# Performance work log

Hardware: AMD Instinct MI355X
Metric: run time of the kernel (lower is better)

The kernel has to match this reference:

```python
import jax, jax.numpy as jnp
import numpy as np

H, W, C = 56, 56, 384
WS, SHIFT, HEADS = 7, 3, 12
HEAD_DIM = C // HEADS
SCALE = HEAD_DIM ** (-0.5)
NWIN = (H // WS) * (W // WS)  # 64 windows per image
NTOK = WS * WS                # 49 tokens per window
EPS = 1e-5


def _gen_mask():
    # static shift-window attention mask, computed with numpy (jit-safe constant)
    img = np.zeros((H, W))
    sl = (slice(0, -WS), slice(-WS, -SHIFT), slice(-SHIFT, None))
    cnt = 0
    for hs in sl:
        for ws in sl:
            img[hs, ws] = cnt
            cnt += 1
    mw = img.reshape(H // WS, WS, W // WS, WS).transpose(0, 2, 1, 3).reshape(-1, NTOK)
    diff = mw[:, None, :] - mw[:, :, None]  # (NWIN, NTOK, NTOK)
    return jnp.asarray(np.where(diff != 0, -100.0, 0.0), dtype=jnp.float32)

ATTN_MASK = _gen_mask()


def _layernorm(x, g, b):
    mu = jnp.mean(x, axis=-1, keepdims=True)
    var = jnp.var(x, axis=-1, keepdims=True)
    return (x - mu) * jax.lax.rsqrt(var + EPS) * g + b


def setup_inputs() -> dict:
    key = jax.random.key(0)
    ks = jax.random.split(key, 6)
    s = 0.02
    return {
        "x": jax.random.normal(ks[0], (16, H * W, C), dtype=jnp.float32),
        "ln1_g": jnp.ones((C,), jnp.float32),
        "ln1_b": jnp.zeros((C,), jnp.float32),
        "qkv_w": jax.random.normal(ks[1], (C, 3 * C), jnp.float32) * s,
        "proj_w": jax.random.normal(ks[2], (C, C), jnp.float32) * s,
        "proj_b": jnp.zeros((C,), jnp.float32),
        "ln2_g": jnp.ones((C,), jnp.float32),
        "ln2_b": jnp.zeros((C,), jnp.float32),
        "fc1_w": jax.random.normal(ks[3], (C, 4 * C), jnp.float32) * s,
        "fc1_b": jnp.zeros((4 * C,), jnp.float32),
        "fc2_w": jax.random.normal(ks[4], (4 * C, C), jnp.float32) * s,
        "fc2_b": jnp.zeros((C,), jnp.float32),
    }


def reference(x, ln1_g, ln1_b, qkv_w, proj_w, proj_b, ln2_g, ln2_b, fc1_w, fc1_b, fc2_w, fc2_b):
    B, N, _ = x.shape
    h = x
    y = _layernorm(x, ln1_g, ln1_b).reshape(B, H, W, C)
    # cyclic shift (note: source never rolls back; we match it)
    y = jnp.roll(y, shift=(-SHIFT, -SHIFT), axis=(1, 2))
    # window partition -> (B*NWIN, NTOK, C)
    y = y.reshape(B, H // WS, WS, W // WS, WS, C).transpose(0, 1, 3, 2, 4, 5)
    y = y.reshape(B * NWIN, NTOK, C)
    # qkv (no bias), split heads
    qkv = (y @ qkv_w).reshape(B * NWIN, NTOK, 3, HEADS, HEAD_DIM)
    qkv = qkv.transpose(2, 0, 3, 1, 4)  # (3, BW, heads, NTOK, hd)
    q, k, v = qkv[0], qkv[1], qkv[2]
    attn = jnp.einsum('whnd,whmd->whnm', q, k) * SCALE  # (BW, heads, NTOK, NTOK)
    attn = attn.reshape(B, NWIN, HEADS, NTOK, NTOK) + ATTN_MASK[None, :, None]
    attn = jax.nn.softmax(attn.reshape(B * NWIN, HEADS, NTOK, NTOK), axis=-1)
    o = jnp.einsum('whnm,whmd->whnd', attn, v)
    o = o.transpose(0, 2, 1, 3).reshape(B * NWIN, NTOK, C)
    o = o @ proj_w + proj_b
    # window reverse -> (B, N, C)
    o = o.reshape(B, H // WS, W // WS, WS, WS, C).transpose(0, 1, 3, 2, 4, 5)
    o = o.reshape(B, N, C)
    x1 = h + o
    # MLP (GELU after both fc1 and fc2, as in source)
    m = _layernorm(x1, ln2_g, ln2_b)
    m = jax.nn.gelu(m @ fc1_w + fc1_b, approximate=False)
    m = jax.nn.gelu(m @ fc2_w + fc2_b, approximate=False)
    return x1 + m
```

## Files before the change

kernel.cpp:

```cpp
#include <hip/hip_runtime.h>
#include <hip/hip_bf16.h>
#include <cstdint>
#include <cstddef>

#define C_DIM   384
#define NIMG    3136
#define MROWS   50176
#define QK_SCALE 0.17677669529663687f

using bf16x8 = __attribute__((ext_vector_type(8))) short;
using f32x4  = __attribute__((ext_vector_type(4))) float;

__device__ __forceinline__ short f2bf(float f) {
  union { float f; uint32_t u; } v; v.f = f;
  uint32_t r = (v.u + 0x7fffu + ((v.u >> 16) & 1u)) >> 16;
  return (short)(uint16_t)r;
}

__device__ __forceinline__ float bf2f(short s) {
  union { uint32_t u; float f; } v; v.u = ((uint32_t)(uint16_t)s) << 16;
  return v.f;
}

__device__ __forceinline__ void async_copy16(const void* g, void* l) {
  __builtin_amdgcn_global_load_lds(
      (const __attribute__((address_space(1))) void*)g,
      (__attribute__((address_space(3))) void*)l, 16, 0, 0);
}

__device__ __forceinline__ float gelu_fast(float x) {
  float x2 = x * x;
  float u = fmaf(0.0356774081f, x2, 0.7978845608f);
  float e = exp2f(x * u * 2.8853900818f);
  float r = __builtin_amdgcn_rcpf(e + 1.0f);
  return fmaf(-x, r, x);
}

__global__ __launch_bounds__(256) void transpose_cast(
    const float* __restrict__ w, short* __restrict__ wt, int K, int N) {
  int idx = blockIdx.x * 256 + threadIdx.x;
  if (idx >= K * N) return;
  int k = idx / N;
  int n = idx - k * N;
  wt[(size_t)n * K + k] = f2bf(w[idx]);
}

template <typename IN>
__global__ __launch_bounds__(256) void ln_kernel(
    const IN* __restrict__ x, const float* __restrict__ g,
    const float* __restrict__ b, short* __restrict__ y, int windowed) {
  int token = blockIdx.x * 4 + (threadIdx.x >> 6);
  int lane = threadIdx.x & 63;
  size_t src;
  if (windowed) {
    int bw = token / 49;
    int tt = token - bw * 49;
    int bb = bw >> 6, w = bw & 63;
    int hs = (w >> 3) * 7 + tt / 7 + 3; if (hs >= 56) hs -= 56;
    int ws = (w & 7) * 7 + (tt % 7) + 3; if (ws >= 56) ws -= 56;
    src = (size_t)(bb * NIMG + hs * 56 + ws) * C_DIM;
  } else {
    src = (size_t)token * C_DIM;
  }
  const IN* xr = x + src;
  float v[6];
  float s = 0.f;
#pragma unroll
  for (int i = 0; i < 6; ++i) {
    if constexpr (sizeof(IN) == 4) v[i] = (float)xr[lane + i * 64];
    else v[i] = bf2f((short)xr[lane + i * 64]);
    s += v[i];
  }
#pragma unroll
  for (int m = 1; m < 64; m <<= 1) s += __shfl_xor(s, m);
  float mu = s * (1.0f / 384.0f);
  float var = 0.f;
#pragma unroll
  for (int i = 0; i < 6; ++i) { float d = v[i] - mu; var += d * d; }
#pragma unroll
  for (int m = 1; m < 64; m <<= 1) var += __shfl_xor(var, m);
  float rstd = rsqrtf(var * (1.0f / 384.0f) + 1e-5f);
  short* yr = y + (size_t)token * C_DIM;
#pragma unroll
  for (int i = 0; i < 6; ++i) {
    int c = lane + i * 64;
    yr[c] = f2bf((v[i] - mu) * rstd * g[c] + b[c]);
  }
}

template <int EPI>
__device__ __forceinline__ void gemm_epilogue(
    f32x4 (&acc)[4][4], void* Out, const float* bias, const void* resid,
    int N, int m0, int n0, int wm, int wn, int lrow, int quad) {
#pragma unroll
  for (int i = 0; i < 4; ++i) {
#pragma unroll
    for (int r = 0; r < 4; ++r) {
      int row = m0 + wm * 64 + i * 16 + quad * 4 + r;
      if (EPI == 1) {
        int bw = row / 49;
        int tt = row - bw * 49;
        int bb = bw >> 6, w = bw & 63;
        int nimg = ((w >> 3) * 7 + tt / 7) * 56 + (w & 7) * 7 + (tt % 7);
        size_t obase = ((size_t)(bb * NIMG + nimg)) * C_DIM;
#pragma unroll
        for (int j = 0; j < 4; ++j) {
          int col = n0 + wn * 64 + j * 16 + lrow;
          size_t oi = obase + col;
          ((short*)Out)[oi] =
              f2bf(acc[i][j][r] + bias[col] + ((const float*)resid)[oi]);
        }
      } else {
#pragma unroll
        for (int j = 0; j < 4; ++j) {
          int col = n0 + wn * 64 + j * 16 + lrow;
          float v = acc[i][j][r];
          if (EPI == 0) {
            ((short*)Out)[(size_t)row * N + col] = f2bf(v);
          } else if (EPI == 2) {
            ((short*)Out)[(size_t)row * N + col] = f2bf(gelu_fast(v + bias[col]));
          } else {
            size_t oi = (size_t)row * C_DIM + col;
            ((float*)Out)[oi] =
                bf2f(((const short*)resid)[oi]) + gelu_fast(v + bias[col]);
          }
        }
      }
    }
  }
}

__device__ __forceinline__ void grid_decode(int nby, int& m0, int& n0) {
  const int wg = (int)blockIdx.x;
  const int swz = (wg & 7) * ((int)gridDim.x >> 3) + (wg >> 3);
  const int mb = swz / nby;
  const int nb = swz - mb * nby;
  m0 = mb * 128;
  n0 = nb * 128;
}

template <int EPI>
__global__ __launch_bounds__(256, 4) void gemm_pipe32_kernel(
    const short* __restrict__ A, const short* __restrict__ Bt,
    void* __restrict__ Out, const float* __restrict__ bias,
    const void* __restrict__ resid, int M, int N, int K, int nby) {
  __shared__ __align__(16) short lds[2][128 * 32 * 2];
  const int t = threadIdx.x;
  const int wave = t >> 6, lane = t & 63;
  const int lrow = lane & 15, quad = lane >> 4;
  const int wm = wave & 1, wn = wave >> 1;
  int m0, n0;
  grid_decode(nby, m0, n0);

  f32x4 acc[4][4] = {};
  const int srow = t >> 2;
  const int spos = t & 3;
  const int nt = K >> 5;

  auto stage = [&](int buf, int k0) {
    short* la = &lds[buf][0];
    short* lb = la + 128 * 32;
#pragma unroll
    for (int i = 0; i < 2; ++i) {
      int row = i * 64 + srow;
      int ca = spos ^ ((row >> 1) & 3);
      async_copy16(A + (size_t)(m0 + row) * K + k0 + ca * 8,
                   la + (i * 64 + wave * 16) * 32);
      async_copy16(Bt + (size_t)(n0 + row) * K + k0 + ca * 8,
                   lb + (i * 64 + wave * 16) * 32);
    }
  };

  auto compute = [&](int buf) {
    short* ldsA = &lds[buf][0];
    short* ldsB = ldsA + 128 * 32;
    bf16x8 af[4], bfr[4];
#pragma unroll
    for (int i = 0; i < 4; ++i) {
      int ra = wm * 64 + i * 16 + lrow;
      af[i] = *(const bf16x8*)(ldsA + ra * 32 + ((quad ^ ((ra >> 1) & 3)) * 8));
      int rb = wn * 64 + i * 16 + lrow;
      bfr[i] = *(const bf16x8*)(ldsB + rb * 32 + ((quad ^ ((rb >> 1) & 3)) * 8));
    }
    __builtin_amdgcn_s_setprio(1);
#pragma unroll
    for (int i = 0; i < 4; ++i)
#pragma unroll
      for (int j = 0; j < 4; ++j)
        acc[i][j] = __builtin_amdgcn_mfma_f32_16x16x32_bf16(af[i], bfr[j],
                                                            acc[i][j], 0, 0, 0);
    __builtin_amdgcn_s_setprio(0);
  };

  stage(0, 0);
  for (int kt = 0; kt < nt; ++kt) {
    __builtin_amdgcn_sched_barrier(0);
    if (kt + 1 < nt) {
      stage((kt + 1) & 1, (kt + 1) * 32);
      asm volatile("s_waitcnt vmcnt(4)" ::: "memory");
    } else {
      asm volatile("s_waitcnt vmcnt(0)" ::: "memory");
    }
    __builtin_amdgcn_s_barrier();
    __builtin_amdgcn_sched_barrier(0);
    compute(kt & 1);
    __builtin_amdgcn_sched_barrier(0);
    __builtin_amdgcn_s_barrier();
  }
  gemm_epilogue<EPI>(acc, Out, bias, resid, N, m0, n0, wm, wn, lrow, quad);
}

template <int EPI>
__global__ __launch_bounds__(256, 2) void gemm_pipe64_kernel(
    const short* __restrict__ A, const short* __restrict__ Bt,
    void* __restrict__ Out, const float* __restrict__ bias,
    const void* __restrict__ resid, int M, int N, int K, int nby) {
  __shared__ __align__(16) short lds[2][128 * 64 * 2];
  const int t = threadIdx.x;
  const int wave = t >> 6, lane = t & 63;
  const int lrow = lane & 15, quad = lane >> 4;
  const int wm = wave & 1, wn = wave >> 1;
  int m0, n0;
  grid_decode(nby, m0, n0);

  f32x4 acc[4][4] = {};
  const int srow = t >> 3;
  const int spos = t & 7;
  const int nt = K >> 6;

  auto stage = [&](int buf, int k0) {
    short* la = &lds[buf][0];
    short* lb = la + 128 * 64;
#pragma unroll
    for (int i = 0; i < 4; ++i) {
      int row = i * 32 + srow;
      int ca = spos ^ (row & 7);
      async_copy16(A + (size_t)(m0 + row) * K + k0 + ca * 8,
                   la + (i * 32 + wave * 8) * 64);
      async_copy16(Bt + (size_t)(n0 + row) * K + k0 + ca * 8,
                   lb + (i * 32 + wave * 8) * 64);
    }
  };

  auto compute = [&](int buf) {
    short* ldsA = &lds[buf][0];
    short* ldsB = ldsA + 128 * 64;
#pragma unroll
    for (int ks = 0; ks < 2; ++ks) {
      const int cb = ks * 4;
      bf16x8 af[4], bfr[4];
#pragma unroll
      for (int i = 0; i < 4; ++i) {
        int ra = wm * 64 + i * 16 + lrow;
        af[i] = *(const bf16x8*)(ldsA + ra * 64 + (((cb + quad) ^ (ra & 7)) * 8));
        int rb = wn * 64 + i * 16 + lrow;
        bfr[i] = *(const bf16x8*)(ldsB + rb * 64 + (((cb + quad) ^ (rb & 7)) * 8));
      }
      __builtin_amdgcn_s_setprio(1);
#pragma unroll
      for (int i = 0; i < 4; ++i)
#pragma unroll
        for (int j = 0; j < 4; ++j)
          acc[i][j] = __builtin_amdgcn_mfma_f32_16x16x32_bf16(af[i], bfr[j],
                                                              acc[i][j], 0, 0, 0);
      __builtin_amdgcn_s_setprio(0);
    }
  };

  stage(0, 0);
  for (int kt = 0; kt < nt; ++kt) {
    __builtin_amdgcn_sched_barrier(0);
    if (kt + 1 < nt) {
      stage((kt + 1) & 1, (kt + 1) * 64);
      asm volatile("s_waitcnt vmcnt(8)" ::: "memory");
    } else {
      asm volatile("s_waitcnt vmcnt(0)" ::: "memory");
    }
    __builtin_amdgcn_s_barrier();
    __builtin_amdgcn_sched_barrier(0);
    compute(kt & 1);
    __builtin_amdgcn_sched_barrier(0);
    __builtin_amdgcn_s_barrier();
  }
  gemm_epilogue<EPI>(acc, Out, bias, resid, N, m0, n0, wm, wn, lrow, quad);
}

__global__ __launch_bounds__(256) void attn_kernel(
    const short* __restrict__ qkv, short* __restrict__ o) {
  __shared__ __align__(16) short plds[4][64 * 72];
  const int wavei = threadIdx.x >> 6;
  const int lane = threadIdx.x & 63;
  const int gw = blockIdx.x * 4 + wavei;
  const int bw = gw / 12;
  const int h = gw - bw * 12;
  const int w = bw & 63;
  const int lrow = lane & 15, quad = lane >> 4;
  const short* base = qkv + (size_t)bw * 49 * 1152 + h * 32;

  bf16x8 qf[4], kf[4];
#pragma unroll
  for (int i = 0; i < 4; ++i) {
    int tq = i * 16 + lrow;
    const short* p = base + (size_t)tq * 1152 + quad * 8;
    qf[i] = *(const bf16x8*)p;
    kf[i] = *(const bf16x8*)(p + 384);
  }
  f32x4 sa[4][4] = {};
#pragma unroll
  for (int i = 0; i < 4; ++i)
#pragma unroll
    for (int j = 0; j < 4; ++j)
      sa[i][j] = __builtin_amdgcn_mfma_f32_16x16x32_bf16(qf[i], kf[j], sa[i][j], 0, 0, 0);

  int tl = lane < 49 ? lane : 0;
  int rr = tl / 7, cc = tl - rr * 7;
  int hs = (w >> 3) * 7 + rr;
  int ws = (w & 7) * 7 + cc;
  int id = (hs < 49 ? 0 : (hs < 53 ? 3 : 6)) + (ws < 49 ? 0 : (ws < 53 ? 1 : 2));

  int idn[4], idm[4][4];
#pragma unroll
  for (int j = 0; j < 4; ++j) idn[j] = __shfl(id, j * 16 + lrow);
#pragma unroll
  for (int i = 0; i < 4; ++i)
#pragma unroll
    for (int r = 0; r < 4; ++r) idm[i][r] = __shfl(id, i * 16 + quad * 4 + r);

#pragma unroll
  for (int i = 0; i < 4; ++i)
#pragma unroll
    for (int j = 0; j < 4; ++j)
#pragma unroll
      for (int r = 0; r < 4; ++r) {
        float v = sa[i][j][r] * QK_SCALE + (idm[i][r] == idn[j] ? 0.f : -100.f);
        sa[i][j][r] = (j * 16 + lrow < 49) ? v : -1e30f;
      }

#pragma unroll
  for (int i = 0; i < 4; ++i)
#pragma unroll
    for (int r = 0; r < 4; ++r) {
      float mx = -1e30f;
#pragma unroll
      for (int j = 0; j < 4; ++j) mx = fmaxf(mx, sa[i][j][r]);
#pragma unroll
      for (int m = 1; m < 16; m <<= 1) mx = fmaxf(mx, __shfl_xor(mx, m));
      float sum = 0.f;
#pragma unroll
      for (int j = 0; j < 4; ++j) {
        float e = exp2f((sa[i][j][r] - mx) * 1.44269504f);
        sa[i][j][r] = e;
        sum += e;
      }
#pragma unroll
      for (int m = 1; m < 16; m <<= 1) sum += __shfl_xor(sum, m);
      float inv = 1.0f / sum;
#pragma unroll
      for (int j = 0; j < 4; ++j) sa[i][j][r] *= inv;
    }

  short* pw = plds[wavei];
#pragma unroll
  for (int i = 0; i < 4; ++i)
#pragma unroll
    for (int r = 0; r < 4; ++r)
#pragma unroll
      for (int j = 0; j < 4; ++j)
        pw[(i * 16 + quad * 4 + r) * 72 + j * 16 + lrow] = f2bf(sa[i][j][r]);

  f32x4 oa[4][2] = {};
#pragma unroll
  for (int kk = 0; kk < 2; ++kk) {
    bf16x8 vf[2];
#pragma unroll
    for (int j2 = 0; j2 < 2; ++j2) {
#pragma unroll
      for (int jj = 0; jj < 8; ++jj) {
        int n = kk * 32 + quad * 8 + jj;
        vf[j2][jj] = (n < 49)
            ? base[768 + (size_t)n * 1152 + j2 * 16 + lrow]
            : (short)0;
      }
    }
#pragma unroll
    for (int i = 0; i < 4; ++i) {
      bf16x8 pf = *(const bf16x8*)(pw + (i * 16 + lrow) * 72 + kk * 32 + quad * 8);
#pragma unroll
      for (int j2 = 0; j2 < 2; ++j2)
        oa[i][j2] = __builtin_amdgcn_mfma_f32_16x16x32_bf16(pf, vf[j2], oa[i][j2], 0, 0, 0);
    }
  }

#pragma unroll
  for (int i = 0; i < 4; ++i)
#pragma unroll
    for (int j2 = 0; j2 < 2; ++j2)
#pragma unroll
      for (int r = 0; r < 4; ++r) {
        int m = i * 16 + quad * 4 + r;
        if (m < 49)
          o[((size_t)bw * 49 + m) * 384 + h * 32 + j2 * 16 + lrow] = f2bf(oa[i][j2][r]);
      }
}

extern "C" void kernel_launch(void* const* d_in, const int* in_sizes, int n_in,
                              void* d_out, int out_size, void* d_ws, size_t ws_size,
                              hipStream_t stream) {
  const float* x      = (const float*)d_in[0];
  const float* ln1_g  = (const float*)d_in[1];
  const float* ln1_b  = (const float*)d_in[2];
  const float* qkv_w  = (const float*)d_in[3];
  const float* proj_w = (const float*)d_in[4];
  const float* proj_b = (const float*)d_in[5];
  const float* ln2_g  = (const float*)d_in[6];
  const float* ln2_b  = (const float*)d_in[7];
  const float* fc1_w  = (const float*)d_in[8];
  const float* fc1_b  = (const float*)d_in[9];
  const float* fc2_w  = (const float*)d_in[10];
  const float* fc2_b  = (const float*)d_in[11];
  float* out = (float*)d_out;

  char* ws = (char*)d_ws;
  auto alloc = [&](size_t bytes) {
    char* p = ws;
    ws += (bytes + 255) & ~(size_t)255;
    return p;
  };
  short* qkv_wT  = (short*)alloc((size_t)1152 * 384 * 2);
  short* proj_wT = (short*)alloc((size_t)384 * 384 * 2);
  short* fc1_wT  = (short*)alloc((size_t)1536 * 384 * 2);
  short* fc2_wT  = (short*)alloc((size_t)384 * 1536 * 2);
  short* bufA    = (short*)alloc((size_t)MROWS * 384 * 2);
  short* x1      = (short*)alloc((size_t)MROWS * 384 * 2);
  short* bufB    = (short*)alloc((size_t)MROWS * 1536 * 2);

  transpose_cast<<<(384 * 1152) / 256, 256, 0, stream>>>(qkv_w, qkv_wT, 384, 1152);
  transpose_cast<<<(384 * 384) / 256, 256, 0, stream>>>(proj_w, proj_wT, 384, 384);
  transpose_cast<<<(384 * 1536) / 256, 256, 0, stream>>>(fc1_w, fc1_wT, 384, 1536);
  transpose_cast<<<(1536 * 384) / 256, 256, 0, stream>>>(fc2_w, fc2_wT, 1536, 384);

  ln_kernel<float><<<MROWS / 4, 256, 0, stream>>>(x, ln1_g, ln1_b, bufA, 1);

  gemm_pipe32_kernel<0><<<392 * 9, 256, 0, stream>>>(bufA, qkv_wT, bufB, nullptr,
                                                     nullptr, MROWS, 1152, 384, 9);

  attn_kernel<<<3072, 256, 0, stream>>>(bufB, bufA);

  gemm_pipe32_kernel<1><<<392 * 3, 256, 0, stream>>>(bufA, proj_wT, x1, proj_b,
                                                     x, MROWS, 384, 384, 3);

  ln_kernel<short><<<MROWS / 4, 256, 0, stream>>>(x1, ln2_g, ln2_b, bufA, 0);

  gemm_pipe32_kernel<2><<<392 * 12, 256, 0, stream>>>(bufA, fc1_wT, bufB, fc1_b,
                                                      nullptr, MROWS, 1536, 384, 12);

  gemm_pipe64_kernel<3><<<392 * 3, 256, 0, stream>>>(bufB, fc2_wT, out, fc2_b,
                                                     x1, MROWS, 384, 1536, 3);
}
```

Measured before the change: 519.7 us.

## Stage V through LDS transposed in attention and use pipe32 GEMM for fc2

The attention kernel now loads each V row with vectorized 16-byte global reads, writes it transposed into a per-wave LDS tile, and builds the MFMA B operands from LDS. This replaces the strided, scalar, predicated global loads used before. Separately, the fc2 GEMM switches from the 64-wide K-tile pipelined kernel to the 32-wide one, and the 64-wide kernel is deleted. The change adds LDS usage per block and a transposed LDS write pattern that may hit bank conflicts. The fc2 change trades a deeper K tile for the configuration used by the other GEMMs.

```diff
diff --git a/kernel.cpp b/kernel.cpp
--- a/kernel.cpp
+++ b/kernel.cpp
@@ -210,84 +210,10 @@
   gemm_epilogue<EPI>(acc, Out, bias, resid, N, m0, n0, wm, wn, lrow, quad);
 }
 
-template <int EPI>
-__global__ __launch_bounds__(256, 2) void gemm_pipe64_kernel(
-    const short* __restrict__ A, const short* __restrict__ Bt,
-    void* __restrict__ Out, const float* __restrict__ bias,
-    const void* __restrict__ resid, int M, int N, int K, int nby) {
-  __shared__ __align__(16) short lds[2][128 * 64 * 2];
-  const int t = threadIdx.x;
-  const int wave = t >> 6, lane = t & 63;
-  const int lrow = lane & 15, quad = lane >> 4;
-  const int wm = wave & 1, wn = wave >> 1;
-  int m0, n0;
-  grid_decode(nby, m0, n0);
-
-  f32x4 acc[4][4] = {};
-  const int srow = t >> 3;
-  const int spos = t & 7;
-  const int nt = K >> 6;
-
-  auto stage = [&](int buf, int k0) {
-    short* la = &lds[buf][0];
-    short* lb = la + 128 * 64;
-#pragma unroll
-    for (int i = 0; i < 4; ++i) {
-      int row = i * 32 + srow;
-      int ca = spos ^ (row & 7);
-      async_copy16(A + (size_t)(m0 + row) * K + k0 + ca * 8,
-                   la + (i * 32 + wave * 8) * 64);
-      async_copy16(Bt + (size_t)(n0 + row) * K + k0 + ca * 8,
-                   lb + (i * 32 + wave * 8) * 64);
-    }
-  };
-
-  auto compute = [&](int buf) {
-    short* ldsA = &lds[buf][0];
-    short* ldsB = ldsA + 128 * 64;
-#pragma unroll
-    for (int ks = 0; ks < 2; ++ks) {
-      const int cb = ks * 4;
-      bf16x8 af[4], bfr[4];
-#pragma unroll
-      for (int i = 0; i < 4; ++i) {
-        int ra = wm * 64 + i * 16 + lrow;
-        af[i] = *(const bf16x8*)(ldsA + ra * 64 + (((cb + quad) ^ (ra & 7)) * 8));
-        int rb = wn * 64 + i * 16 + lrow;
-        bfr[i] = *(const bf16x8*)(ldsB + rb * 64 + (((cb + quad) ^ (rb & 7)) * 8));
-      }
-      __builtin_amdgcn_s_setprio(1);
-#pragma unroll
-      for (int i = 0; i < 4; ++i)
-#pragma unroll
-        for (int j = 0; j < 4; ++j)
-          acc[i][j] = __builtin_amdgcn_mfma_f32_16x16x32_bf16(af[i], bfr[j],
-                                                              acc[i][j], 0, 0, 0);
-      __builtin_amdgcn_s_setprio(0);
-    }
-  };
-
-  stage(0, 0);
-  for (int kt = 0; kt < nt; ++kt) {
-    __builtin_amdgcn_sched_barrier(0);
-    if (kt + 1 < nt) {
-      stage((kt + 1) & 1, (kt + 1) * 64);
-      asm volatile("s_waitcnt vmcnt(8)" ::: "memory");
-    } else {
-      asm volatile("s_waitcnt vmcnt(0)" ::: "memory");
-    }
-    __builtin_amdgcn_s_barrier();
-    __builtin_amdgcn_sched_barrier(0);
-    compute(kt & 1);
-    __builtin_amdgcn_sched_barrier(0);
-    __builtin_amdgcn_s_barrier();
-  }
-  gemm_epilogue<EPI>(acc, Out, bias, resid, N, m0, n0, wm, wn, lrow, quad);
-}
-
 __global__ __launch_bounds__(256) void attn_kernel(
     const short* __restrict__ qkv, short* __restrict__ o) {
   __shared__ __align__(16) short plds[4][64 * 72];
+  __shared__ __align__(16) short vlds[4][32 * 72];
   const int wavei = threadIdx.x >> 6;
   const int lane = threadIdx.x & 63;
   const int gw = blockIdx.x * 4 + wavei;
@@ -305,6 +231,22 @@
     qf[i] = *(const bf16x8*)p;
     kf[i] = *(const bf16x8*)(p + 384);
   }
+
+  short* vw = vlds[wavei];
+  {
+    bf16x8 vrow[4] = {};
+    if (lane < 49) {
+      const short* vp = base + 768 + (size_t)lane * 1152;
+#pragma unroll
+      for (int c = 0; c < 4; ++c) vrow[c] = *(const bf16x8*)(vp + c * 8);
+    }
+#pragma unroll
+    for (int c = 0; c < 4; ++c)
+#pragma unroll
+      for (int jj = 0; jj < 8; ++jj)
+        vw[(c * 8 + jj) * 72 + lane] = vrow[c][jj];
+  }
+
   f32x4 sa[4][4] = {};
 #pragma unroll
   for (int i = 0; i < 4; ++i)
@@ -373,15 +315,8 @@
   for (int kk = 0; kk < 2; ++kk) {
     bf16x8 vf[2];
 #pragma unroll
-    for (int j2 = 0; j2 < 2; ++j2) {
-#pragma unroll
-      for (int jj = 0; jj < 8; ++jj) {
-        int n = kk * 32 + quad * 8 + jj;
-        vf[j2][jj] = (n < 49)
-            ? base[768 + (size_t)n * 1152 + j2 * 16 + lrow]
-            : (short)0;
-      }
-    }
+    for (int j2 = 0; j2 < 2; ++j2)
+      vf[j2] = *(const bf16x8*)(vw + (j2 * 16 + lrow) * 72 + kk * 32 + quad * 8);
 #pragma unroll
     for (int i = 0; i < 4; ++i) {
       bf16x8 pf = *(const bf16x8*)(pw + (i * 16 + lrow) * 72 + kk * 32 + quad * 8);
@@ -454,6 +389,6 @@
   gemm_pipe32_kernel<2><<<392 * 12, 256, 0, stream>>>(bufA, fc1_wT, bufB, fc1_b,
                                                       nullptr, MROWS, 1536, 384, 12);
 
-  gemm_pipe64_kernel<3><<<392 * 3, 256, 0, stream>>>(bufB, fc2_wT, out, fc2_b,
+  gemm_pipe32_kernel<3><<<392 * 3, 256, 0, stream>>>(bufB, fc2_wT, out, fc2_b,
                                                      x1, MROWS, 384, 1536, 3);
 }
```

Result: slower. 538.9 us (+3.7%).
